# Performance work log

Hardware: AMD Instinct MI355X
Metric: run time of the kernel (lower is better)

## Reference

```python
import jax, jax.numpy as jnp
import numpy as np
from jax import lax

B, C, H, W = 2, 3, 512, 512
K = 8                 # kernel_size (= value_patch_size)
G = H // K            # token grid = 64
L = G * G             # 4096 tokens
FD = 128              # feature_dim
PD = C * K * K        # 192 rgb patch dim
MD = PD + FD          # 320 matching token dim
DD = 256              # matching_descriptor_dim
TOPK = 16             # attention_top_k (= reranker_top_k)
RH = 128              # reranker hidden
TEMP = 1.0
NEG = -1e9


def _to_tokens(img):
    # [B,C,H,W] -> [B,L,C*K*K], channel-major patch layout (torch unfold order)
    b = img.shape[0]
    x = img.reshape(b, C, G, K, G, K).transpose(0, 2, 4, 1, 3, 5)
    return x.reshape(b, L, PD)


def _from_tokens(tok):
    # inverse of _to_tokens (non-overlapping fold)
    b = tok.shape[0]
    x = tok.reshape(b, G, G, C, K, K).transpose(0, 3, 1, 4, 2, 5)
    return x.reshape(b, C, H, W)


def setup_inputs() -> dict:
    key = jax.random.key(0)
    ks = jax.random.split(key, 9)
    s = lambda d: 1.0 / np.sqrt(d)
    return {
        "image": jax.random.normal(ks[0], (B, C, H, W), jnp.float32),
        "features": jax.random.normal(ks[1], (B, FD, G, G), jnp.float32),
        "token_mask": jax.random.randint(ks[2], (B, L), 0, 2, jnp.int32),
        "W_desc": jax.random.normal(ks[3], (MD, DD), jnp.float32) * s(MD),
        "Wq_rr": jax.random.normal(ks[4], (MD, RH), jnp.float32) * s(MD),
        "Wk_rr": jax.random.normal(ks[5], (MD, RH), jnp.float32) * s(MD),
        "W1": jax.random.normal(ks[6], (2 * RH + 3, RH), jnp.float32) * s(2 * RH + 3),
        "b1": jnp.zeros((RH,), jnp.float32),
        "W2": jax.random.normal(ks[7], (RH, 1), jnp.float32) * s(RH),
        "b2": jnp.zeros((1,), jnp.float32),
    }


def reference(image, features, token_mask, W_desc, Wq_rr, Wk_rr, W1, b1, W2, b2):
    rgb_tok = _to_tokens(image)                                   # [B,L,192]
    feat_tok = features.reshape(B, FD, L).transpose(0, 2, 1)      # [B,L,128]
    match = jnp.concatenate([rgb_tok, feat_tok], axis=-1)          # [B,L,320]

    # stage-1 matching: descriptor GEMM + scaled dot-product logits
    desc = match @ W_desc                                          # [B,L,256]
    scale = 1.0 / (np.sqrt(DD) * TEMP)
    logits = jnp.einsum("bqd,bkd->bqk", desc, desc) * scale        # [B,L,L]
    key_invalid = token_mask.astype(logits.dtype)                  # 1 = hole
    logits = logits + NEG * key_invalid[:, None, :]

    # top-k candidate selection per query token
    top_logits, top_idx = lax.top_k(logits, TOPK)                  # [B,L,TOPK]

    gather = jax.vmap(lambda m, i: m[i])                            # per-batch gather
    cand = gather(match, top_idx)                                  # [B,L,TOPK,320]

    # relative coordinates on the token grid, normalized
    ys, xs = jnp.meshgrid(jnp.arange(G), jnp.arange(G), indexing="ij")
    pos = jnp.stack([ys.reshape(-1), xs.reshape(-1)], -1).astype(jnp.float32) / G  # [L,2]
    rel = pos[top_idx] - pos[None, :, None, :]                      # [B,L,TOPK,2]

    # reranker MLP over (query, candidate) pairs
    qf = match @ Wq_rr                                              # [B,L,RH]
    kf = cand @ Wk_rr                                               # [B,L,TOPK,RH]
    feats = jnp.concatenate(
        [qf[:, :, None, :] * kf,
         jnp.abs(qf[:, :, None, :] - kf),
         top_logits[..., None],
         rel], axis=-1)                                             # [B,L,TOPK,2RH+3]
    score = (jax.nn.gelu(feats @ W1 + b1, approximate=False) @ W2 + b2)[..., 0]
    refined = top_logits + score                                    # [B,L,TOPK]

    weights = jax.nn.softmax(refined, axis=-1)                      # [B,L,TOPK]

    # gather value patches (value_source='rgb') and blend
    vcand = gather(rgb_tok, top_idx)                                # [B,L,TOPK,192]
    out_tok = jnp.einsum("blk,blkp->blp", weights, vcand)           # [B,L,192]
    out_img = _from_tokens(out_tok)                                 # [B,C,H,W]

    # fusion_mode='replace': replace hole pixels, keep valid pixels
    pix_mask = jnp.repeat(jnp.repeat(token_mask.reshape(B, G, G), K, 1), K, 2)
    pix_mask = pix_mask[:, None, :, :]                              # [B,1,H,W]
    return jnp.where(pix_mask > 0, out_img, image)
```

## Files before the change

### kernel.cpp

```cpp
#include <hip/hip_runtime.h>
#include <hip/hip_bf16.h>
#include <math.h>

#define BB 2
#define CC 3
#define HH 512
#define WW 512
#define GG 64
#define LL 4096
#define FDIM 128
#define PDIM 192
#define MDIM 320
#define DDIM 256
#define TOPK 16
#define RHID 128
#define SCALE (1.0f/16.0f)

#define NQ2 8
#define CHK3 1024
#define TOKG 16
#define TKT 32

__global__ void k_copy_init(const float* __restrict__ img, float* __restrict__ out,
                            int* __restrict__ counts) {
    int i = blockIdx.x * blockDim.x + threadIdx.x;
    if (i < 2 * BB) counts[i] = 0;
    int n4 = BB * CC * HH * WW / 4;
    const float4* s = (const float4*)img;
    float4* d = (float4*)out;
    for (int j = i; j < n4; j += gridDim.x * blockDim.x) d[j] = s[j];
}

__global__ void k_build(const float* __restrict__ img, const float* __restrict__ feat,
                        float* __restrict__ match) {
    int bl = blockIdx.x;
    int b = bl >> 12, l = bl & (LL - 1);
    int gy = l >> 6, gx = l & 63;
    int p = threadIdx.x;
    float v;
    if (p < PDIM) {
        int c = p >> 6, ky = (p >> 3) & 7, kx = p & 7;
        v = img[((b * CC + c) * HH + gy * 8 + ky) * WW + gx * 8 + kx];
    } else {
        v = feat[(b * FDIM + (p - PDIM)) * LL + l];
    }
    match[(size_t)bl * MDIM + p] = v;
}

__global__ void k_compact(const int* __restrict__ mask, int* __restrict__ qlist,
                          int* __restrict__ klist, int* __restrict__ counts) {
    int bl = blockIdx.x * blockDim.x + threadIdx.x;
    if (bl >= BB * LL) return;
    int b = bl >> 12, l = bl & (LL - 1);
    if (mask[bl] > 0) {
        int s = atomicAdd(&counts[b], 1);
        qlist[b * LL + s] = l;
    } else {
        int s = atomicAdd(&counts[BB + b], 1);
        klist[b * LL + s] = l;
    }
}

__global__ __launch_bounds__(256) void k_gemm2(const float* __restrict__ match,
        const float* __restrict__ Wd, const float* __restrict__ Wq,
        const float* __restrict__ Wk,
        float* __restrict__ desc, float* __restrict__ qkf) {
    __shared__ float sm[TOKG * MDIM];
    int base = blockIdx.x * TOKG;
    int t = threadIdx.x;
    for (int i = t; i < TOKG * MDIM; i += 256) sm[i] = match[(size_t)base * MDIM + i];
    __syncthreads();
    const float4* sm4 = (const float4*)sm;
    const float* W1p = (t < 128) ? Wq : Wk;
    int c1 = t & 127;
    float acc0[TOKG], acc1[TOKG];
#pragma unroll
    for (int tt = 0; tt < TOKG; ++tt) { acc0[tt] = 0.f; acc1[tt] = 0.f; }
    for (int m = 0; m < MDIM; m += 4) {
        float w00 = Wd[(m+0)*DDIM + t], w01 = Wd[(m+1)*DDIM + t];
        float w02 = Wd[(m+2)*DDIM + t], w03 = Wd[(m+3)*DDIM + t];
        float w10 = W1p[(m+0)*RHID + c1], w11 = W1p[(m+1)*RHID + c1];
        float w12 = W1p[(m+2)*RHID + c1], w13 = W1p[(m+3)*RHID + c1];
        int mg = m >> 2;
#pragma unroll
        for (int tt = 0; tt < TOKG; ++tt) {
            float4 s = sm4[tt * (MDIM/4) + mg];
            acc0[tt] += s.x*w00 + s.y*w01 + s.z*w02 + s.w*w03;
            acc1[tt] += s.x*w10 + s.y*w11 + s.z*w12 + s.w*w13;
        }
    }
#pragma unroll
    for (int tt = 0; tt < TOKG; ++tt) {
        desc[(size_t)(base+tt)*DDIM + t] = acc0[tt];
        qkf [(size_t)(base+tt)*DDIM + t] = acc1[tt];
    }
}

__global__ __launch_bounds__(256) void k_gatherkT(const float* __restrict__ desc,
        const int* __restrict__ klist, const int* __restrict__ counts,
        float* __restrict__ kdesc_t) {
    int b = blockIdx.y;
    int vcnt = counts[BB + b];
    int kt = blockIdx.x * TKT;
    if (kt >= vcnt) return;
    int nk = min(TKT, vcnt - kt);
    __shared__ float sm[TKT][DDIM + 1];
    int t = threadIdx.x;
    for (int r = (t >> 6); r < nk; r += 4) {
        int src = klist[b * LL + kt + r];
        const float4* s = (const float4*)(desc + ((size_t)b * LL + src) * DDIM);
        float4 v = s[t & 63];
        int d0 = (t & 63) * 4;
        sm[r][d0] = v.x; sm[r][d0+1] = v.y; sm[r][d0+2] = v.z; sm[r][d0+3] = v.w;
    }
    __syncthreads();
    float* outb = kdesc_t + (size_t)b * DDIM * LL;
    int kk = t & 31;
    for (int d = (t >> 5); d < DDIM; d += 8) {
        if (kk < nk) outb[(size_t)d * LL + kt + kk] = sm[kk][d];
    }
}

__global__ __launch_bounds__(256, 4) void k_topk4(const float* __restrict__ desc,
        const float* __restrict__ kdt,
        const int* __restrict__ qlist, const int* __restrict__ klist,
        const int* __restrict__ counts,
        float* __restrict__ tval2, int* __restrict__ tidx2) {
    int b = blockIdx.z;
    int kb = blockIdx.y;
    int cnt  = counts[b];
    int vcnt = counts[BB + b];
    int i0 = blockIdx.x * NQ2;
    if (i0 >= cnt) return;
    int nq = min(NQ2, cnt - i0);
    int t = threadIdx.x;
    int lane = t & 63, w = t >> 6;

    __shared__ float sq[NQ2 * DDIM];
    __shared__ float lc[NQ2][CHK3];

#pragma unroll
    for (int qi = 0; qi < NQ2; ++qi) {
        int qtok = qlist[b * LL + i0 + min(qi, nq - 1)];
        sq[qi * DDIM + t] = desc[((size_t)b * LL + qtok) * DDIM + t];
    }
    __syncthreads();

    int khalf = (vcnt + 1) >> 1;
    int kstart = kb * khalf;
    int kend = min(vcnt, kstart + khalf);

    float tva = -INFINITY, tvb = -INFINITY;
    int   tia = 0x7fffffff, tib = 0x7fffffff;

    const float4* sq4 = (const float4*)sq;
    const float* kbase = kdt + (size_t)b * DDIM * LL;
    const int* klb = klist + b * LL;

    int nch = (kend > kstart) ? (kend - kstart + CHK3 - 1) / CHK3 : 0;
    for (int ch = 0; ch < nch; ++ch) {
        int base = kstart + ch * CHK3;
        int k0 = base + 4 * t;
        int k0c = min(k0, LL - 4);

        float acc[NQ2][4];
#pragma unroll
        for (int qi = 0; qi < NQ2; ++qi)
#pragma unroll
            for (int r = 0; r < 4; ++r) acc[qi][r] = 0.f;

#pragma unroll 2
        for (int db = 0; db < DDIM / 4; ++db) {
            float4 qv[NQ2];
#pragma unroll
            for (int qi = 0; qi < NQ2; ++qi) qv[qi] = sq4[qi * (DDIM/4) + db];
#pragma unroll
            for (int dd = 0; dd < 4; ++dd) {
                float4 kx = *(const float4*)(kbase + (size_t)(db * 4 + dd) * LL + k0c);
#pragma unroll
                for (int qi = 0; qi < NQ2; ++qi) {
                    float sv = (dd == 0) ? qv[qi].x : (dd == 1) ? qv[qi].y
                             : (dd == 2) ? qv[qi].z : qv[qi].w;
                    acc[qi][0] += sv * kx.x;
                    acc[qi][1] += sv * kx.y;
                    acc[qi][2] += sv * kx.z;
                    acc[qi][3] += sv * kx.w;
                }
            }
        }
        __syncthreads();
#pragma unroll
        for (int qi = 0; qi < NQ2; ++qi) {
            float4 o;
            o.x = (k0 + 0 < kend) ? acc[qi][0] * SCALE : -INFINITY;
            o.y = (k0 + 1 < kend) ? acc[qi][1] * SCALE : -INFINITY;
            o.z = (k0 + 2 < kend) ? acc[qi][2] * SCALE : -INFINITY;
            o.w = (k0 + 3 < kend) ? acc[qi][3] * SCALE : -INFINITY;
            *(float4*)&lc[qi][4 * t] = o;
        }
        __syncthreads();

        auto select_q = [&](float& tv, int& ti, int qi) {
            for (int j = 0; j < CHK3 / 64; ++j) {
                int p = j * 64 + lane;
                int gk = base + p;
                float v = lc[qi][p];
                int kidx = (gk < kend) ? klb[gk] : 0x7fffffff;
                float thrv = __shfl(tv, 15);
                int   thri = __shfl(ti, 15);
                bool pass = (v > thrv) || (v == thrv && kidx < thri);
                unsigned long long mball = __ballot(pass);
                while (mball) {
                    int src = __ffsll(mball) - 1;
                    float vv = __shfl(v, src);
                    int   ii = __shfl(kidx, src);
                    bool beat = (vv > tv) || (vv == tv && ii < ti);
                    float pv = __shfl_up(tv, 1);
                    int   pi = __shfl_up(ti, 1);
                    bool beatp = (lane > 0) && ((vv > pv) || (vv == pv && ii < pi));
                    if (lane < 16 && beat) { tv = beatp ? pv : vv; ti = beatp ? pi : ii; }
                    mball &= mball - 1;
                }
            }
        };
        select_q(tva, tia, 2 * w + 0);
        select_q(tvb, tib, 2 * w + 1);
    }

#pragma unroll
    for (int qq = 0; qq < 2; ++qq) {
        int qi = w * 2 + qq;
        float tv = qq ? tvb : tva;
        int   ti = qq ? tib : tia;
        if (qi < nq && lane < 16) {
            size_t o = (((size_t)b * LL + i0 + qi) * 2 + kb) * TOPK + lane;
            tval2[o] = tv;
            tidx2[o] = ti;
        }
    }
}

__global__ __launch_bounds__(128) void k_mlp(const float* __restrict__ match,
        const float* __restrict__ qkf,
        const float* __restrict__ tval2, const int* __restrict__ tidx2,
        const int* __restrict__ qlist, const int* __restrict__ counts,
        const float* __restrict__ W1, const float* __restrict__ b1,
        const float* __restrict__ W2, const float* __restrict__ b2,
        float* __restrict__ out) {
    int b = blockIdx.y;
    int i = blockIdx.x;
    if (i >= counts[b]) return;
    int q = qlist[b * LL + i];
    size_t slot = (size_t)b * LL + i;
    int t = threadIdx.x;

    __shared__ float mv[32];
    __shared__ int   mi[32];
    __shared__ float qfv[RHID];
    __shared__ float kfv[TOPK][RHID];
    __shared__ float tl[TOPK];
    __shared__ int   tix[TOPK];
    __shared__ float r0[TOPK], r1[TOPK];
    __shared__ float red[TOPK][2];
    __shared__ float wgt[TOPK];
    __shared__ float w2s[RHID];
    __shared__ __align__(16) float2 pkpa[RHID][18];

    if (t < 32) {
        size_t o = (slot * 2 + (t >> 4)) * TOPK + (t & 15);
        mv[t] = tval2[o];
        mi[t] = tidx2[o];
    }
    __syncthreads();
    if (t < 32) {
        float v = mv[t]; int ii = mi[t];
        int rank = 0;
        for (int u = 0; u < 32; ++u) {
            float vu = mv[u]; int iu = mi[u];
            rank += ((vu > v) || (vu == v && (iu < ii || (iu == ii && u < t)))) ? 1 : 0;
        }
        if (rank < TOPK) {
            tl[rank] = v;
            int kidx = ii;
            if (kidx < 0 || kidx >= LL) kidx = 0;
            tix[rank] = kidx;
        }
    }
    __syncthreads();

    int gyq = q >> 6, gxq = q & 63;
    if (t < TOPK) {
        int kidx = tix[t];
        int gyk = kidx >> 6, gxk = kidx & 63;
        r0[t] = (float)(gyk - gyq) * (1.0f / GG);
        r1[t] = (float)(gxk - gxq) * (1.0f / GG);
    }
    qfv[t] = qkf[((size_t)b * LL + q) * DDIM + t];
    w2s[t] = W2[t];
    for (int i2 = t; i2 < TOPK * RHID; i2 += 128) {
        int kk = i2 >> 7, d = i2 & (RHID - 1);
        kfv[kk][d] = qkf[((size_t)b * LL + tix[kk]) * DDIM + RHID + d];
    }
    __syncthreads();
    {
        float qv = qfv[t];
#pragma unroll
        for (int kk = 0; kk < TOPK; ++kk) {
            float kv = kfv[kk][t];
            pkpa[t][kk] = make_float2(qv * kv, fabsf(qv - kv));
        }
    }
    __syncthreads();

    int h = t;
    float acc[TOPK];
#pragma unroll
    for (int kk = 0; kk < TOPK; ++kk) acc[kk] = 0.f;
    for (int j = 0; j < RHID; ++j) {
        const float4* row4 = (const float4*)(&pkpa[j][0]);
        float w1a = W1[j * RHID + h];
        float w1b = W1[(RHID + j) * RHID + h];
#pragma unroll
        for (int m = 0; m < 8; ++m) {
            float4 r = row4[m];
            acc[2*m]   += r.x * w1a + r.y * w1b;
            acc[2*m+1] += r.z * w1a + r.w * w1b;
        }
    }
    float wl  = W1[256 * RHID + h];
    float wr0 = W1[257 * RHID + h];
    float wr1 = W1[258 * RHID + h];
    float bb1 = b1[h];
    float w2v = w2s[h];
    float sc[TOPK];
#pragma unroll
    for (int kk = 0; kk < TOPK; ++kk) {
        float x = acc[kk] + tl[kk] * wl + r0[kk] * wr0 + r1[kk] * wr1 + bb1;
        float g = 0.5f * x * (1.0f + erff(x * 0.70710678118654752f));
        sc[kk] = g * w2v;
    }
    int lane = t & 63, wv = t >> 6;
#pragma unroll
    for (int kk = 0; kk < TOPK; ++kk) {
        float v = sc[kk];
        for (int off = 32; off > 0; off >>= 1) v += __shfl_down(v, off);
        if (lane == 0) red[kk][wv] = v;
    }
    __syncthreads();
    if (t < TOPK) {
        float score = red[t][0] + red[t][1] + b2[0];
        float refined = tl[t] + score;
        float m = refined;
        for (int off = 8; off > 0; off >>= 1) m = fmaxf(m, __shfl_xor(m, off, 16));
        float e = expf(refined - m);
        float s = e;
        for (int off = 8; off > 0; off >>= 1) s += __shfl_xor(s, off, 16);
        wgt[t] = e / s;
    }
    __syncthreads();
    for (int p = t; p < PDIM; p += 128) {
        float o = 0.f;
#pragma unroll
        for (int kk = 0; kk < TOPK; ++kk)
            o += wgt[kk] * match[((size_t)b * LL + tix[kk]) * MDIM + p];
        int c = p >> 6, ky = (p >> 3) & 7, kx = p & 7;
        out[((b * CC + c) * HH + gyq * 8 + ky) * WW + gxq * 8 + kx] = o;
    }
}

extern "C" void kernel_launch(void* const* d_in, const int* in_sizes, int n_in,
                              void* d_out, int out_size, void* d_ws, size_t ws_size,
                              hipStream_t stream) {
    const float* image    = (const float*)d_in[0];
    const float* features = (const float*)d_in[1];
    const int*   tmask    = (const int*)d_in[2];
    const float* W_desc   = (const float*)d_in[3];
    const float* Wq       = (const float*)d_in[4];
    const float* Wk       = (const float*)d_in[5];
    const float* W1       = (const float*)d_in[6];
    const float* b1       = (const float*)d_in[7];
    const float* W2       = (const float*)d_in[8];
    const float* b2       = (const float*)d_in[9];
    float* out = (float*)d_out;

    float* ws    = (float*)d_ws;
    float* match = ws;
    float* desc  = match + (size_t)BB * LL * MDIM;
    float* qkf   = desc  + (size_t)BB * LL * DDIM;
    float* kdt   = qkf   + (size_t)BB * LL * DDIM;
    float* tval2 = kdt   + (size_t)BB * DDIM * LL;
    int*   tidx2 = (int*)(tval2 + (size_t)BB * LL * 2 * TOPK);
    int*   qlist = tidx2 + (size_t)BB * LL * 2 * TOPK;
    int*   klist = qlist + BB * LL;
    int*   counts = klist + BB * LL;

    k_copy_init<<<1024, 256, 0, stream>>>(image, out, counts);
    k_build<<<BB * LL, MDIM, 0, stream>>>(image, features, match);
    k_compact<<<(BB * LL + 255) / 256, 256, 0, stream>>>(tmask, qlist, klist, counts);
    k_gemm2<<<BB * LL / TOKG, 256, 0, stream>>>(match, W_desc, Wq, Wk, desc, qkf);
    k_gatherkT<<<dim3(LL / TKT, BB), 256, 0, stream>>>(desc, klist, counts, kdt);
    k_topk4<<<dim3(LL / NQ2, 2, BB), 256, 0, stream>>>(desc, kdt, qlist, klist,
                                                       counts, tval2, tidx2);
    k_mlp<<<dim3(LL, BB), 128, 0, stream>>>(match, qkf, tval2, tidx2, qlist, counts,
                                            W1, b1, W2, b2, out);
}
```

Before: 475.8 us.

## Process more queries per block in top-k scoring and reranker MLP kernels

The top-k kernel now computes 16 queries per block against each key chunk instead of 8. This halves how often the transposed key descriptors are loaded, and selection runs in two passes through the shared logits buffer. The reranker MLP is rewritten to handle 4 queries per 256-thread block with a register tile of 4 candidates by 8 hidden units per thread. W1 rows are read as float4 and reused across candidates, replacing the per-query 128-thread layout. The cost is higher register pressure (occupancy hint lowered to 3) and extra syncs between the selection passes.

Measured after the change: 535.8 us. 1.13x slower.

```diff
diff --git a/kernel.cpp b/kernel.cpp
--- a/kernel.cpp
+++ b/kernel.cpp
@@ -16,10 +16,11 @@
 #define RHID 128
 #define SCALE (1.0f/16.0f)
 
-#define NQ2 8
+#define NQ3 16
 #define CHK3 1024
 #define TOKG 16
 #define TKT 32
+#define NQM 4
 
 __global__ void k_copy_init(const float* __restrict__ img, float* __restrict__ out,
                             int* __restrict__ counts) {
@@ -121,7 +122,7 @@
     }
 }
 
-__global__ __launch_bounds__(256, 4) void k_topk4(const float* __restrict__ desc,
+__global__ __launch_bounds__(256, 3) void k_topk5(const float* __restrict__ desc,
         const float* __restrict__ kdt,
         const int* __restrict__ qlist, const int* __restrict__ klist,
         const int* __restrict__ counts,
@@ -130,17 +131,17 @@
     int kb = blockIdx.y;
     int cnt  = counts[b];
     int vcnt = counts[BB + b];
-    int i0 = blockIdx.x * NQ2;
+    int i0 = blockIdx.x * NQ3;
     if (i0 >= cnt) return;
-    int nq = min(NQ2, cnt - i0);
+    int nq = min(NQ3, cnt - i0);
     int t = threadIdx.x;
     int lane = t & 63, w = t >> 6;
 
-    __shared__ float sq[NQ2 * DDIM];
-    __shared__ float lc[NQ2][CHK3];
-
-#pragma unroll
-    for (int qi = 0; qi < NQ2; ++qi) {
+    __shared__ float sq[NQ3 * DDIM];
+    __shared__ float lc[8][CHK3];
+
+#pragma unroll 1
+    for (int qi = 0; qi < NQ3; ++qi) {
         int qtok = qlist[b * LL + i0 + min(qi, nq - 1)];
         sq[qi * DDIM + t] = desc[((size_t)b * LL + qtok) * DDIM + t];
     }
@@ -150,8 +151,8 @@
     int kstart = kb * khalf;
     int kend = min(vcnt, kstart + khalf);
 
-    float tva = -INFINITY, tvb = -INFINITY;
-    int   tia = 0x7fffffff, tib = 0x7fffffff;
+    float tv0 = -INFINITY, tv1 = -INFINITY, tv2 = -INFINITY, tv3 = -INFINITY;
+    int   ti0 = 0x7fffffff, ti1 = 0x7fffffff, ti2 = 0x7fffffff, ti3 = 0x7fffffff;
 
     const float4* sq4 = (const float4*)sq;
     const float* kbase = kdt + (size_t)b * DDIM * LL;
@@ -163,48 +164,32 @@
         int k0 = base + 4 * t;
         int k0c = min(k0, LL - 4);
 
-        float acc[NQ2][4];
-#pragma unroll
-        for (int qi = 0; qi < NQ2; ++qi)
+        float acc[NQ3][4];
+#pragma unroll
+        for (int qi = 0; qi < NQ3; ++qi)
 #pragma unroll
             for (int r = 0; r < 4; ++r) acc[qi][r] = 0.f;
 
-#pragma unroll 2
         for (int db = 0; db < DDIM / 4; ++db) {
-            float4 qv[NQ2];
-#pragma unroll
-            for (int qi = 0; qi < NQ2; ++qi) qv[qi] = sq4[qi * (DDIM/4) + db];
-#pragma unroll
-            for (int dd = 0; dd < 4; ++dd) {
-                float4 kx = *(const float4*)(kbase + (size_t)(db * 4 + dd) * LL + k0c);
-#pragma unroll
-                for (int qi = 0; qi < NQ2; ++qi) {
-                    float sv = (dd == 0) ? qv[qi].x : (dd == 1) ? qv[qi].y
-                             : (dd == 2) ? qv[qi].z : qv[qi].w;
-                    acc[qi][0] += sv * kx.x;
-                    acc[qi][1] += sv * kx.y;
-                    acc[qi][2] += sv * kx.z;
-                    acc[qi][3] += sv * kx.w;
-                }
+            float4 kx0 = *(const float4*)(kbase + (size_t)(db*4+0) * LL + k0c);
+            float4 kx1 = *(const float4*)(kbase + (size_t)(db*4+1) * LL + k0c);
+            float4 kx2 = *(const float4*)(kbase + (size_t)(db*4+2) * LL + k0c);
+            float4 kx3 = *(const float4*)(kbase + (size_t)(db*4+3) * LL + k0c);
+#pragma unroll
+            for (int qi = 0; qi < NQ3; ++qi) {
+                float4 qv = sq4[qi * (DDIM/4) + db];
+                acc[qi][0] += qv.x*kx0.x + qv.y*kx1.x + qv.z*kx2.x + qv.w*kx3.x;
+                acc[qi][1] += qv.x*kx0.y + qv.y*kx1.y + qv.z*kx2.y + qv.w*kx3.y;
+                acc[qi][2] += qv.x*kx0.z + qv.y*kx1.z + qv.z*kx2.z + qv.w*kx3.z;
+                acc[qi][3] += qv.x*kx0.w + qv.y*kx1.w + qv.z*kx2.w + qv.w*kx3.w;
             }
         }
-        __syncthreads();
-#pragma unroll
-        for (int qi = 0; qi < NQ2; ++qi) {
-            float4 o;
-            o.x = (k0 + 0 < kend) ? acc[qi][0] * SCALE : -INFINITY;
-            o.y = (k0 + 1 < kend) ? acc[qi][1] * SCALE : -INFINITY;
-            o.z = (k0 + 2 < kend) ? acc[qi][2] * SCALE : -INFINITY;
-            o.w = (k0 + 3 < kend) ? acc[qi][3] * SCALE : -INFINITY;
-            *(float4*)&lc[qi][4 * t] = o;
-        }
-        __syncthreads();
-
-        auto select_q = [&](float& tv, int& ti, int qi) {
+
+        auto select_q = [&](float& tv, int& ti, int lrow) {
             for (int j = 0; j < CHK3 / 64; ++j) {
                 int p = j * 64 + lane;
                 int gk = base + p;
-                float v = lc[qi][p];
+                float v = lc[lrow][p];
                 int kidx = (gk < kend) ? klb[gk] : 0x7fffffff;
                 float thrv = __shfl(tv, 15);
                 int   thri = __shfl(ti, 15);
@@ -223,24 +208,56 @@
                 }
             }
         };
-        select_q(tva, tia, 2 * w + 0);
-        select_q(tvb, tib, 2 * w + 1);
-    }
-
-#pragma unroll
-    for (int qq = 0; qq < 2; ++qq) {
-        int qi = w * 2 + qq;
-        float tv = qq ? tvb : tva;
-        int   ti = qq ? tib : tia;
-        if (qi < nq && lane < 16) {
-            size_t o = (((size_t)b * LL + i0 + qi) * 2 + kb) * TOPK + lane;
-            tval2[o] = tv;
-            tidx2[o] = ti;
-        }
-    }
-}
-
-__global__ __launch_bounds__(128) void k_mlp(const float* __restrict__ match,
+
+        __syncthreads();
+#pragma unroll
+        for (int qi = 0; qi < 8; ++qi) {
+            float4 o;
+            o.x = (k0 + 0 < kend) ? acc[qi][0] * SCALE : -INFINITY;
+            o.y = (k0 + 1 < kend) ? acc[qi][1] * SCALE : -INFINITY;
+            o.z = (k0 + 2 < kend) ? acc[qi][2] * SCALE : -INFINITY;
+            o.w = (k0 + 3 < kend) ? acc[qi][3] * SCALE : -INFINITY;
+            *(float4*)&lc[qi][4 * t] = o;
+        }
+        __syncthreads();
+        select_q(tv0, ti0, 2 * w + 0);
+        select_q(tv1, ti1, 2 * w + 1);
+
+        __syncthreads();
+#pragma unroll
+        for (int qi = 8; qi < 16; ++qi) {
+            float4 o;
+            o.x = (k0 + 0 < kend) ? acc[qi][0] * SCALE : -INFINITY;
+            o.y = (k0 + 1 < kend) ? acc[qi][1] * SCALE : -INFINITY;
+            o.z = (k0 + 2 < kend) ? acc[qi][2] * SCALE : -INFINITY;
+            o.w = (k0 + 3 < kend) ? acc[qi][3] * SCALE : -INFINITY;
+            *(float4*)&lc[qi - 8][4 * t] = o;
+        }
+        __syncthreads();
+        select_q(tv2, ti2, 2 * w + 0);
+        select_q(tv3, ti3, 2 * w + 1);
+    }
+
+    if (lane < 16) {
+        int qs[4] = {2*w, 2*w + 1, 8 + 2*w, 8 + 2*w + 1};
+        float tvs[4] = {tv0, tv1, tv2, tv3};
+        int   tis[4] = {ti0, ti1, ti2, ti3};
+#pragma unroll
+        for (int e = 0; e < 4; ++e) {
+            if (qs[e] < nq) {
+                size_t o = (((size_t)b * LL + i0 + qs[e]) * 2 + kb) * TOPK + lane;
+                tval2[o] = tvs[e];
+                tidx2[o] = tis[e];
+            }
+        }
+    }
+}
+
+__device__ __forceinline__ float gelu_f(float x) {
+    return 0.5f * x * (1.0f + erff(x * 0.70710678118654752f));
+}
+
+__global__ __launch_bounds__(256, 4) void k_mlp2(const float* __restrict__ match,
         const float* __restrict__ qkf,
         const float* __restrict__ tval2, const int* __restrict__ tidx2,
         const int* __restrict__ qlist, const int* __restrict__ counts,
@@ -248,121 +265,149 @@
         const float* __restrict__ W2, const float* __restrict__ b2,
         float* __restrict__ out) {
     int b = blockIdx.y;
-    int i = blockIdx.x;
-    if (i >= counts[b]) return;
-    int q = qlist[b * LL + i];
-    size_t slot = (size_t)b * LL + i;
+    int cnt = counts[b];
+    int i0 = blockIdx.x * NQM;
+    if (i0 >= cnt) return;
     int t = threadIdx.x;
-
-    __shared__ float mv[32];
-    __shared__ int   mi[32];
-    __shared__ float qfv[RHID];
-    __shared__ float kfv[TOPK][RHID];
-    __shared__ float tl[TOPK];
-    __shared__ int   tix[TOPK];
-    __shared__ float r0[TOPK], r1[TOPK];
-    __shared__ float red[TOPK][2];
-    __shared__ float wgt[TOPK];
-    __shared__ float w2s[RHID];
-    __shared__ __align__(16) float2 pkpa[RHID][18];
-
-    if (t < 32) {
-        size_t o = (slot * 2 + (t >> 4)) * TOPK + (t & 15);
-        mv[t] = tval2[o];
-        mi[t] = tidx2[o];
-    }
-    __syncthreads();
-    if (t < 32) {
-        float v = mv[t]; int ii = mi[t];
+    int ql = t >> 6;
+    int lane = t & 63;
+    int rt = lane >> 4;
+    int ht = lane & 15;
+    int h0 = ht * 8;
+    int k0 = rt * 4;
+
+    __shared__ float mv[NQM][32];
+    __shared__ int   mi[NQM][32];
+    __shared__ float tl[NQM][16];
+    __shared__ int   tix[NQM][16];
+    __shared__ float rr0[NQM][16], rr1[NQM][16];
+    __shared__ int   qtok[NQM];
+    __shared__ float qf[NQM][128];
+    __shared__ float kf[64][132];
+    __shared__ float wgt[NQM][16];
+
+    if (t < NQM) qtok[t] = qlist[b * LL + min(i0 + t, cnt - 1)];
+    if (t < NQM * 32) {
+        int q = t >> 5, u = t & 31;
+        size_t o = (((size_t)b * LL + min(i0 + q, cnt - 1)) * 2 + (u >> 4)) * TOPK + (u & 15);
+        mv[q][u] = tval2[o];
+        mi[q][u] = tidx2[o];
+    }
+    __syncthreads();
+    if (t < NQM * 32) {
+        int q = t >> 5, u = t & 31;
+        float v = mv[q][u]; int ii = mi[q][u];
         int rank = 0;
-        for (int u = 0; u < 32; ++u) {
-            float vu = mv[u]; int iu = mi[u];
-            rank += ((vu > v) || (vu == v && (iu < ii || (iu == ii && u < t)))) ? 1 : 0;
+#pragma unroll 1
+        for (int x = 0; x < 32; ++x) {
+            float vx = mv[q][x]; int ix = mi[q][x];
+            rank += ((vx > v) || (vx == v && (ix < ii || (ix == ii && x < u)))) ? 1 : 0;
         }
         if (rank < TOPK) {
-            tl[rank] = v;
-            int kidx = ii;
-            if (kidx < 0 || kidx >= LL) kidx = 0;
-            tix[rank] = kidx;
-        }
-    }
-    __syncthreads();
-
-    int gyq = q >> 6, gxq = q & 63;
-    if (t < TOPK) {
-        int kidx = tix[t];
-        int gyk = kidx >> 6, gxk = kidx & 63;
-        r0[t] = (float)(gyk - gyq) * (1.0f / GG);
-        r1[t] = (float)(gxk - gxq) * (1.0f / GG);
-    }
-    qfv[t] = qkf[((size_t)b * LL + q) * DDIM + t];
-    w2s[t] = W2[t];
-    for (int i2 = t; i2 < TOPK * RHID; i2 += 128) {
-        int kk = i2 >> 7, d = i2 & (RHID - 1);
-        kfv[kk][d] = qkf[((size_t)b * LL + tix[kk]) * DDIM + RHID + d];
-    }
-    __syncthreads();
+            int kidx = (ii < 0 || ii >= LL) ? 0 : ii;
+            tl[q][rank] = v;
+            tix[q][rank] = kidx;
+            int qt = qtok[q];
+            rr0[q][rank] = (float)((kidx >> 6) - (qt >> 6)) * (1.0f / GG);
+            rr1[q][rank] = (float)((kidx & 63) - (qt & 63)) * (1.0f / GG);
+        }
+    }
+    __syncthreads();
+    for (int idx = t; idx < NQM * 128; idx += 256) {
+        int q = idx >> 7, d = idx & 127;
+        qf[q][d] = qkf[((size_t)b * LL + qtok[q]) * DDIM + d];
+    }
+    for (int idx = t; idx < 64 * 128; idx += 256) {
+        int row = idx >> 7, d = idx & 127;
+        kf[row][d] = qkf[((size_t)b * LL + tix[row >> 4][row & 15]) * DDIM + 128 + d];
+    }
+    __syncthreads();
+
+    float acc[4][8];
+#pragma unroll
+    for (int i = 0; i < 4; ++i)
+#pragma unroll
+        for (int h = 0; h < 8; ++h) acc[i][h] = 0.f;
+
+    const float4* W14 = (const float4*)W1;
+    const float* qfr = qf[ql];
+    const float* kfr0 = &kf[ql * 16 + k0][0];
+    for (int j = 0; j < 128; ++j) {
+        float qv = qfr[j];
+        int ca = (j * RHID + h0) >> 2;
+        int cb = ((RHID + j) * RHID + h0) >> 2;
+        float4 wa0 = W14[ca], wa1 = W14[ca + 1];
+        float4 wb0 = W14[cb], wb1 = W14[cb + 1];
+#pragma unroll
+        for (int i = 0; i < 4; ++i) {
+            float kv = kfr0[i * 132 + j];
+            float pa = qv * kv;
+            float pb = fabsf(qv - kv);
+            acc[i][0] += pa * wa0.x + pb * wb0.x;
+            acc[i][1] += pa * wa0.y + pb * wb0.y;
+            acc[i][2] += pa * wa0.z + pb * wb0.z;
+            acc[i][3] += pa * wa0.w + pb * wb0.w;
+            acc[i][4] += pa * wa1.x + pb * wb1.x;
+            acc[i][5] += pa * wa1.y + pb * wb1.y;
+            acc[i][6] += pa * wa1.z + pb * wb1.z;
+            acc[i][7] += pa * wa1.w + pb * wb1.w;
+        }
+    }
+
+    int cl = (256 * RHID + h0) >> 2;
+    int cr0 = (257 * RHID + h0) >> 2;
+    int cr1 = (258 * RHID + h0) >> 2;
+    float4 wl0 = W14[cl], wl1 = W14[cl + 1];
+    float4 wra = W14[cr0], wrb = W14[cr0 + 1];
+    float4 wsa = W14[cr1], wsb = W14[cr1 + 1];
+    float4 bb0 = ((const float4*)b1)[h0 >> 2], bb1v = ((const float4*)b1)[(h0 >> 2) + 1];
+    float4 w20 = ((const float4*)W2)[h0 >> 2], w21 = ((const float4*)W2)[(h0 >> 2) + 1];
+    float b2v = b2[0];
+
+    float scv0, scv1, scv2, scv3;
     {
-        float qv = qfv[t];
-#pragma unroll
-        for (int kk = 0; kk < TOPK; ++kk) {
-            float kv = kfv[kk][t];
-            pkpa[t][kk] = make_float2(qv * kv, fabsf(qv - kv));
-        }
-    }
-    __syncthreads();
-
-    int h = t;
-    float acc[TOPK];
-#pragma unroll
-    for (int kk = 0; kk < TOPK; ++kk) acc[kk] = 0.f;
-    for (int j = 0; j < RHID; ++j) {
-        const float4* row4 = (const float4*)(&pkpa[j][0]);
-        float w1a = W1[j * RHID + h];
-        float w1b = W1[(RHID + j) * RHID + h];
-#pragma unroll
-        for (int m = 0; m < 8; ++m) {
-            float4 r = row4[m];
-            acc[2*m]   += r.x * w1a + r.y * w1b;
-            acc[2*m+1] += r.z * w1a + r.w * w1b;
-        }
-    }
-    float wl  = W1[256 * RHID + h];
-    float wr0 = W1[257 * RHID + h];
-    float wr1 = W1[258 * RHID + h];
-    float bb1 = b1[h];
-    float w2v = w2s[h];
-    float sc[TOPK];
-#pragma unroll
-    for (int kk = 0; kk < TOPK; ++kk) {
-        float x = acc[kk] + tl[kk] * wl + r0[kk] * wr0 + r1[kk] * wr1 + bb1;
-        float g = 0.5f * x * (1.0f + erff(x * 0.70710678118654752f));
-        sc[kk] = g * w2v;
-    }
-    int lane = t & 63, wv = t >> 6;
-#pragma unroll
-    for (int kk = 0; kk < TOPK; ++kk) {
-        float v = sc[kk];
-        for (int off = 32; off > 0; off >>= 1) v += __shfl_down(v, off);
-        if (lane == 0) red[kk][wv] = v;
-    }
-    __syncthreads();
-    if (t < TOPK) {
-        float score = red[t][0] + red[t][1] + b2[0];
-        float refined = tl[t] + score;
+#pragma unroll
+        for (int i = 0; i < 4; ++i) {
+            int k = k0 + i;
+            float tlv = tl[ql][k], r0v = rr0[ql][k], r1v = rr1[ql][k];
+            float s = 0.f;
+            s += gelu_f(acc[i][0] + tlv*wl0.x + r0v*wra.x + r1v*wsa.x + bb0.x) * w20.x;
+            s += gelu_f(acc[i][1] + tlv*wl0.y + r0v*wra.y + r1v*wsa.y + bb0.y) * w20.y;
+            s += gelu_f(acc[i][2] + tlv*wl0.z + r0v*wra.z + r1v*wsa.z + bb0.z) * w20.z;
+            s += gelu_f(acc[i][3] + tlv*wl0.w + r0v*wra.w + r1v*wsa.w + bb0.w) * w20.w;
+            s += gelu_f(acc[i][4] + tlv*wl1.x + r0v*wrb.x + r1v*wsb.x + bb1v.x) * w21.x;
+            s += gelu_f(acc[i][5] + tlv*wl1.y + r0v*wrb.y + r1v*wsb.y + bb1v.y) * w21.y;
+            s += gelu_f(acc[i][6] + tlv*wl1.z + r0v*wrb.z + r1v*wsb.z + bb1v.z) * w21.z;
+            s += gelu_f(acc[i][7] + tlv*wl1.w + r0v*wrb.w + r1v*wsb.w + bb1v.w) * w21.w;
+            s += __shfl_xor(s, 1); s += __shfl_xor(s, 2);
+            s += __shfl_xor(s, 4); s += __shfl_xor(s, 8);
+            if (i == 0) scv0 = s; else if (i == 1) scv1 = s;
+            else if (i == 2) scv2 = s; else scv3 = s;
+        }
+    }
+    if (ht == 0) {
+        wgt[ql][k0 + 0] = scv0;
+        wgt[ql][k0 + 1] = scv1;
+        wgt[ql][k0 + 2] = scv2;
+        wgt[ql][k0 + 3] = scv3;
+    }
+    __syncthreads();
+    if (lane < 16) {
+        float refined = tl[ql][lane] + wgt[ql][lane] + b2v;
         float m = refined;
         for (int off = 8; off > 0; off >>= 1) m = fmaxf(m, __shfl_xor(m, off, 16));
         float e = expf(refined - m);
         float s = e;
         for (int off = 8; off > 0; off >>= 1) s += __shfl_xor(s, off, 16);
-        wgt[t] = e / s;
-    }
-    __syncthreads();
-    for (int p = t; p < PDIM; p += 128) {
+        wgt[ql][lane] = e / s;
+    }
+    __syncthreads();
+    int gyq = qtok[ql] >> 6, gxq = qtok[ql] & 63;
+    for (int p = lane; p < PDIM; p += 64) {
         float o = 0.f;
 #pragma unroll
-        for (int kk = 0; kk < TOPK; ++kk)
-            o += wgt[kk] * match[((size_t)b * LL + tix[kk]) * MDIM + p];
+        for (int k = 0; k < TOPK; ++k)
+            o += wgt[ql][k] * match[((size_t)b * LL + tix[ql][k]) * MDIM + p];
         int c = p >> 6, ky = (p >> 3) & 7, kx = p & 7;
         out[((b * CC + c) * HH + gyq * 8 + ky) * WW + gxq * 8 + kx] = o;
     }
@@ -399,8 +444,8 @@
     k_compact<<<(BB * LL + 255) / 256, 256, 0, stream>>>(tmask, qlist, klist, counts);
     k_gemm2<<<BB * LL / TOKG, 256, 0, stream>>>(match, W_desc, Wq, Wk, desc, qkf);
     k_gatherkT<<<dim3(LL / TKT, BB), 256, 0, stream>>>(desc, klist, counts, kdt);
-    k_topk4<<<dim3(LL / NQ2, 2, BB), 256, 0, stream>>>(desc, kdt, qlist, klist,
+    k_topk5<<<dim3(LL / NQ3, 2, BB), 256, 0, stream>>>(desc, kdt, qlist, klist,
                                                        counts, tval2, tidx2);
-    k_mlp<<<dim3(LL, BB), 128, 0, stream>>>(match, qkf, tval2, tidx2, qlist, counts,
-                                            W1, b1, W2, b2, out);
-}
+    k_mlp2<<<dim3(LL / NQM, BB), 256, 0, stream>>>(match, qkf, tval2, tidx2, qlist,
+                                                   counts, W1, b1, W2, b2, out);
+}
```
